# Kernel optimization log

Measured on AMD Instinct MI355X. Metric: run time of the kernel, lower is better.

## Reference

```python
import jax, jax.numpy as jnp
import numpy as np

B, S, HS = 2, 2048, 2048
H, KVH, D = 8, 1, 256
ROPE_BASE = 10000.0


def _rope_cos_sin(position_ids, dim, base=ROPE_BASE):
    # position_ids: (B, S) int -> cos/sin: (B, S, dim)
    inv_freq = 1.0 / (base ** (jnp.arange(0, dim, 2, dtype=jnp.float32) / dim))
    thetas = position_ids.astype(jnp.float32)[..., None] * inv_freq  # (B,S,dim/2)
    emb = jnp.concatenate([thetas, thetas], axis=-1)  # (B,S,dim)
    return jnp.cos(emb), jnp.sin(emb)


def _rotate_half(x):
    x1, x2 = jnp.split(x, 2, axis=-1)
    return jnp.concatenate([-x2, x1], axis=-1)


def _apply_rope(q, k, cos, sin):
    # q,k: (B,h,S,D); cos,sin: (B,S,D) -> unsqueeze head dim
    cos = cos[:, None, :, :]
    sin = sin[:, None, :, :]
    q_emb = q * cos + _rotate_half(q) * sin
    k_emb = k * cos + _rotate_half(k) * sin
    return q_emb, k_emb


def setup_inputs() -> dict:
    key = jax.random.key(0)
    k0, k1, k2, k3, k4 = jax.random.split(key, 5)
    hidden_states = jax.random.normal(k0, (B, S, HS), jnp.float32)
    # causal additive mask: 0 where j<=i, large negative otherwise
    causal = jnp.tril(jnp.ones((S, S), dtype=bool))
    attention_mask = jnp.where(causal, 0.0, -1e9).astype(jnp.float32)
    attention_mask = jnp.broadcast_to(attention_mask[None, None], (B, 1, S, S))
    position_ids = jnp.broadcast_to(jnp.arange(S, dtype=jnp.int32)[None], (B, S))
    scale = 0.02
    Wq = jax.random.normal(k1, (HS, H * D), jnp.float32) * scale
    Wk = jax.random.normal(k2, (HS, KVH * D), jnp.float32) * scale
    Wv = jax.random.normal(k3, (HS, KVH * D), jnp.float32) * scale
    Wo = jax.random.normal(k4, (H * D, HS), jnp.float32) * scale
    return {"hidden_states": hidden_states, "attention_mask": attention_mask,
            "position_ids": position_ids, "Wq": Wq, "Wk": Wk, "Wv": Wv, "Wo": Wo}


def reference(hidden_states, attention_mask, position_ids, Wq, Wk, Wv, Wo):
    bs, seq_len, _ = hidden_states.shape
    q = (hidden_states @ Wq).reshape(bs, seq_len, H, D).transpose(0, 2, 1, 3)     # (B,H,S,D)
    k = (hidden_states @ Wk).reshape(bs, seq_len, KVH, D).transpose(0, 2, 1, 3)   # (B,KVH,S,D)
    v = (hidden_states @ Wv).reshape(bs, seq_len, KVH, D).transpose(0, 2, 1, 3)
    cos, sin = _rope_cos_sin(position_ids, D)
    q, k = _apply_rope(q, k, cos, sin)
    n_rep = H // KVH
    k = jnp.repeat(k, n_rep, axis=1)  # GQA repeat -> (B,H,S,D)
    v = jnp.repeat(v, n_rep, axis=1)
    scores = jnp.einsum('bhqd,bhkd->bhqk', q, k) / jnp.sqrt(jnp.float32(D))
    scores = scores + attention_mask
    attn = jax.nn.softmax(scores.astype(jnp.float32), axis=-1).astype(q.dtype)
    out = jnp.einsum('bhqk,bhkd->bhqd', attn, v)            # (B,H,S,D)
    out = out.transpose(0, 2, 1, 3).reshape(bs, seq_len, H * D)
    return out @ Wo
```

## Files before the change

kernel.cpp:

```cpp
#include <hip/hip_runtime.h>
#include <hip/hip_bf16.h>

typedef __bf16 bf16x8 __attribute__((ext_vector_type(8)));
typedef __bf16 bf16x4 __attribute__((ext_vector_type(4)));
typedef float  f32x4  __attribute__((ext_vector_type(4)));

#define MFMA16(a, b, c) __builtin_amdgcn_mfma_f32_16x16x32_bf16((a), (b), (c), 0, 0, 0)

#define GLOBAL_AS(p) ((const __attribute__((address_space(1))) void*)(p))
#define LDS_AS(p)    ((__attribute__((address_space(3))) void*)(p))

__global__ __launch_bounds__(256) void cvt_bf16_kernel(const float* __restrict__ in,
                                                       __bf16* __restrict__ out)
{
    const int idx = blockIdx.x * 256 + threadIdx.x;
    const float4* p = (const float4*)in + (size_t)idx * 2;
    float4 a = p[0], b = p[1];
    bf16x8 o;
    o[0] = (__bf16)a.x; o[1] = (__bf16)a.y; o[2] = (__bf16)a.z; o[3] = (__bf16)a.w;
    o[4] = (__bf16)b.x; o[5] = (__bf16)b.y; o[6] = (__bf16)b.z; o[7] = (__bf16)b.w;
    ((bf16x8*)out)[idx] = o;
}

__global__ __launch_bounds__(128) void trig_kernel(float2* __restrict__ cs)
{
    const int s = blockIdx.x, i = threadIdx.x;
    const float theta = (float)s * exp2f((float)i * (-13.287712379549449f / 128.f));
    float sn, c;
    sincosf(theta, &sn, &c);
    cs[s * 128 + i] = make_float2(c, sn);
}

__global__ __launch_bounds__(256) void transpose_cvt_kernel(const float* __restrict__ W,
                                                            __bf16* __restrict__ Bt,
                                                            int K, int N)
{
    __shared__ float t[32][33];
    const int n0 = blockIdx.x * 32, k0 = blockIdx.y * 32;
    const int x = threadIdx.x, y = threadIdx.y;
#pragma unroll
    for (int r = 0; r < 4; ++r)
        t[y + r * 8][x] = W[(size_t)(k0 + y + r * 8) * N + n0 + x];
    __syncthreads();
#pragma unroll
    for (int r = 0; r < 4; ++r)
        Bt[(size_t)(n0 + y + r * 8) * K + k0 + x] = (__bf16)t[x][y + r * 8];
}

__global__ __launch_bounds__(256) void vt_kernel(const __bf16* __restrict__ qkv,
                                                 __bf16* __restrict__ vT)
{
    __shared__ __bf16 t[32][33];
    const int s0 = blockIdx.x * 32, d0 = blockIdx.y * 32, b = blockIdx.z;
    const int x = threadIdx.x, y = threadIdx.y;
#pragma unroll
    for (int r = 0; r < 4; ++r)
        t[y + r * 8][x] = qkv[(size_t)(b * 2048 + s0 + y + r * 8) * 2560 + 2304 + d0 + x];
    __syncthreads();
#pragma unroll
    for (int r = 0; r < 4; ++r)
        vT[(size_t)(b * 256 + d0 + y + r * 8) * 2048 + s0 + x] = t[x][y + r * 8];
}

template <typename TC>
__global__ __launch_bounds__(256) void gemm_bt(const __bf16* __restrict__ A,
                                               const __bf16* __restrict__ Bt,
                                               TC* __restrict__ C,
                                               int M, int N, int K)
{
    __shared__ __bf16 As[128 * 32];
    __shared__ __bf16 Bs[128 * 32];

    const int tid  = threadIdx.x;
    const int wave = tid >> 6, lane = tid & 63;
    const int quad = lane >> 4, l16 = lane & 15;
    const int wm = (wave >> 1) * 64, wn = (wave & 1) * 64;
    const int bm = blockIdx.y * 128, bn = blockIdx.x * 128;

    f32x4 acc[4][4] = {};

    for (int k0 = 0; k0 < K; k0 += 32) {
        __syncthreads();
#pragma unroll
        for (int c = 0; c < 2; ++c) {
            const int off = tid * 16 + c * 4096;
            const int row = off >> 6;
            const int kb  = (off & 63) >> 1;
            const __bf16* ga = A  + (size_t)(bm + row) * K + k0 + kb;
            const __bf16* gb = Bt + (size_t)(bn + row) * K + k0 + kb;
            __builtin_amdgcn_global_load_lds(GLOBAL_AS(ga), LDS_AS(As + (off >> 1)), 16, 0, 0);
            __builtin_amdgcn_global_load_lds(GLOBAL_AS(gb), LDS_AS(Bs + (off >> 1)), 16, 0, 0);
        }
        __syncthreads();

        bf16x8 af[4];
#pragma unroll
        for (int mi = 0; mi < 4; ++mi)
            af[mi] = *(const bf16x8*)&As[(wm + mi * 16 + l16) * 32 + quad * 8];
#pragma unroll
        for (int ni = 0; ni < 4; ++ni) {
            bf16x8 bfr = *(const bf16x8*)&Bs[(wn + ni * 16 + l16) * 32 + quad * 8];
#pragma unroll
            for (int mi = 0; mi < 4; ++mi)
                acc[mi][ni] = MFMA16(af[mi], bfr, acc[mi][ni]);
        }
    }
#pragma unroll
    for (int mi = 0; mi < 4; ++mi)
#pragma unroll
        for (int ni = 0; ni < 4; ++ni)
#pragma unroll
            for (int r = 0; r < 4; ++r) {
                int row = bm + wm + mi * 16 + quad * 4 + r;
                int col = bn + wn + ni * 16 + l16;
                C[(size_t)row * N + col] = (TC)acc[mi][ni][r];
            }
}

__global__ __launch_bounds__(256) void rope_kernel(__bf16* __restrict__ qkv,
                                                   const float2* __restrict__ cs)
{
    const int bs = blockIdx.x;
    const int s = bs & 2047;
    const int t = threadIdx.x;
    const float QS = 0.09016843787599907f;

    const int hh = t >> 5, i0 = (t & 31) * 4;
    float2 c0 = cs[s * 128 + i0 + 0], c1 = cs[s * 128 + i0 + 1];
    float2 c2 = cs[s * 128 + i0 + 2], c3 = cs[s * 128 + i0 + 3];

    {
        __bf16* p = qkv + (size_t)bs * 2560 + hh * 256 + i0;
        bf16x4 x1 = *(const bf16x4*)p;
        bf16x4 x2 = *(const bf16x4*)(p + 128);
        bf16x4 o1, o2;
        o1[0] = (__bf16)(((float)x1[0] * c0.x - (float)x2[0] * c0.y) * QS);
        o2[0] = (__bf16)(((float)x2[0] * c0.x + (float)x1[0] * c0.y) * QS);
        o1[1] = (__bf16)(((float)x1[1] * c1.x - (float)x2[1] * c1.y) * QS);
        o2[1] = (__bf16)(((float)x2[1] * c1.x + (float)x1[1] * c1.y) * QS);
        o1[2] = (__bf16)(((float)x1[2] * c2.x - (float)x2[2] * c2.y) * QS);
        o2[2] = (__bf16)(((float)x2[2] * c2.x + (float)x1[2] * c2.y) * QS);
        o1[3] = (__bf16)(((float)x1[3] * c3.x - (float)x2[3] * c3.y) * QS);
        o2[3] = (__bf16)(((float)x2[3] * c3.x + (float)x1[3] * c3.y) * QS);
        *(bf16x4*)p = o1;
        *(bf16x4*)(p + 128) = o2;
    }
    if (t < 32) {
        const int j0 = t * 4;
        float2 d0 = cs[s * 128 + j0 + 0], d1 = cs[s * 128 + j0 + 1];
        float2 d2 = cs[s * 128 + j0 + 2], d3 = cs[s * 128 + j0 + 3];
        __bf16* p = qkv + (size_t)bs * 2560 + 2048 + j0;
        bf16x4 x1 = *(const bf16x4*)p;
        bf16x4 x2 = *(const bf16x4*)(p + 128);
        bf16x4 o1, o2;
        o1[0] = (__bf16)((float)x1[0] * d0.x - (float)x2[0] * d0.y);
        o2[0] = (__bf16)((float)x2[0] * d0.x + (float)x1[0] * d0.y);
        o1[1] = (__bf16)((float)x1[1] * d1.x - (float)x2[1] * d1.y);
        o2[1] = (__bf16)((float)x2[1] * d1.x + (float)x1[1] * d1.y);
        o1[2] = (__bf16)((float)x1[2] * d2.x - (float)x2[2] * d2.y);
        o2[2] = (__bf16)((float)x2[2] * d2.x + (float)x1[2] * d2.y);
        o1[3] = (__bf16)((float)x1[3] * d3.x - (float)x2[3] * d3.y);
        o2[3] = (__bf16)((float)x2[3] * d3.x + (float)x1[3] * d3.y);
        *(bf16x4*)p = o1;
        *(bf16x4*)(p + 128) = o2;
    }
}

__global__ __launch_bounds__(256) void attn_kernel(const __bf16* __restrict__ qkv,
                                                   const __bf16* __restrict__ vTg,
                                                   __bf16* __restrict__ og)
{
    __shared__ __bf16 Ks[64 * 256];
    __shared__ __bf16 Vs[272 * 64];
    __shared__ __bf16 Ps[4][16][68];

    const int b = blockIdx.z, h = blockIdx.y;
    const int qt = (int)gridDim.x - 1 - (int)blockIdx.x;
    const int q0 = qt * 64;
    const int tid  = threadIdx.x;
    const int wave = tid >> 6, lane = tid & 63;
    const int quad = lane >> 4, l16 = lane & 15;
    const int xork = l16 & 7;

    if (tid < 128) {
        bf16x8 one;
#pragma unroll
        for (int e = 0; e < 8; ++e) one[e] = (__bf16)1.0f;
        *(bf16x8*)&Vs[256 * 64 + tid * 8] = one;
    }

    const int qrow = q0 + wave * 16 + l16;
    const __bf16* qptr = qkv + (size_t)(b * 2048 + qrow) * 2560 + h * 256;
    bf16x8 qf[8];
#pragma unroll
    for (int dc = 0; dc < 8; ++dc)
        qf[dc] = *(const bf16x8*)(qptr + dc * 32 + quad * 8);

    f32x4 oacc[17] = {};

    const int kKey0 = tid >> 5;
    const int kC    = (tid & 31) ^ (kKey0 & 7);
    const __bf16* kstage0 = qkv + (size_t)b * 2048 * 2560 + 2048
                          + (size_t)kKey0 * 2560 + kC * 8;
    const int vD0 = tid >> 3;
    const int vC  = (tid & 7) ^ (vD0 & 7);
    const __bf16* vstage0 = vTg + (size_t)b * 256 * 2048 + (size_t)vD0 * 2048 + vC * 8;

    int ckK[8];
#pragma unroll
    for (int dc = 0; dc < 8; ++dc) ckK[dc] = (dc * 4 + quad) ^ xork;
    const int chV0 = quad ^ xork;
    const int chV1 = (4 + quad) ^ xork;

    for (int j0 = 0; j0 <= q0; j0 += 64) {
        __syncthreads();
        const __bf16* kst = kstage0 + (size_t)j0 * 2560;
        const __bf16* vst = vstage0 + j0;
#pragma unroll
        for (int p = 0; p < 8; ++p)
            __builtin_amdgcn_global_load_lds(GLOBAL_AS(kst + (size_t)p * 8 * 2560),
                                             LDS_AS(Ks + tid * 8 + p * 2048), 16, 0, 0);
#pragma unroll
        for (int p = 0; p < 8; ++p)
            __builtin_amdgcn_global_load_lds(GLOBAL_AS(vst + (size_t)p * 32 * 2048),
                                             LDS_AS(Vs + tid * 8 + p * 2048), 16, 0, 0);
        __syncthreads();

        f32x4 sc[4] = {};
#pragma unroll
        for (int nt = 0; nt < 4; ++nt) {
            const __bf16* krow = &Ks[(nt * 16 + l16) * 256];
#pragma unroll
            for (int dc = 0; dc < 8; ++dc) {
                bf16x8 kf = *(const bf16x8*)(krow + ckK[dc] * 8);
                sc[nt] = MFMA16(qf[dc], kf, sc[nt]);
            }
        }
        if (j0 == q0) {
#pragma unroll
            for (int nt = 0; nt < 4; ++nt) {
                int key = j0 + nt * 16 + l16;
#pragma unroll
                for (int r = 0; r < 4; ++r) {
                    int row = q0 + wave * 16 + quad * 4 + r;
                    if (key > row) sc[nt][r] = -1e30f;
                }
            }
        }
#pragma unroll
        for (int nt = 0; nt < 4; ++nt)
#pragma unroll
            for (int r = 0; r < 4; ++r)
                Ps[wave][quad * 4 + r][nt * 16 + l16] = (__bf16)exp2f(sc[nt][r] - 8.f);
        bf16x8 pf0 = *(const bf16x8*)&Ps[wave][l16][quad * 8];
        bf16x8 pf1 = *(const bf16x8*)&Ps[wave][l16][32 + quad * 8];
#pragma unroll
        for (int dt = 0; dt < 17; ++dt) {
            const __bf16* vrow = &Vs[(dt * 16 + l16) * 64];
            bf16x8 vf0 = *(const bf16x8*)(vrow + chV0 * 8);
            bf16x8 vf1 = *(const bf16x8*)(vrow + chV1 * 8);
            oacc[dt] = MFMA16(pf0, vf0, oacc[dt]);
            oacc[dt] = MFMA16(pf1, vf1, oacc[dt]);
        }
    }
    float invl[4];
#pragma unroll
    for (int r = 0; r < 4; ++r) invl[r] = 1.f / oacc[16][r];
#pragma unroll
    for (int dt = 0; dt < 16; ++dt)
#pragma unroll
        for (int r = 0; r < 4; ++r) {
            int row = q0 + wave * 16 + quad * 4 + r;
            int col = h * 256 + dt * 16 + l16;
            og[(size_t)(b * 2048 + row) * 2048 + col] = (__bf16)(oacc[dt][r] * invl[r]);
        }
}

extern "C" void kernel_launch(void* const* d_in, const int* in_sizes, int n_in,
                              void* d_out, int out_size, void* d_ws, size_t ws_size,
                              hipStream_t stream)
{
    (void)in_sizes; (void)n_in; (void)out_size; (void)ws_size;
    const float* hidden = (const float*)d_in[0];
    const float* Wq = (const float*)d_in[3];
    const float* Wk = (const float*)d_in[4];
    const float* Wv = (const float*)d_in[5];
    const float* Wo = (const float*)d_in[6];

    char* ws = (char*)d_ws;
    __bf16* hb    = (__bf16*)(ws);
    __bf16* qkv   = (__bf16*)(ws + (16u << 20));
    __bf16* vTb   = (__bf16*)(ws + (36u << 20));
    __bf16* ob    = (__bf16*)(ws + (38u << 20));
    __bf16* Wqkvt = (__bf16*)(ws + (54u << 20));
    __bf16* Wot   = (__bf16*)(ws + (64u << 20));
    float2* csb   = (float2*)(ws + (72u << 20));
    float* out = (float*)d_out;

    dim3 blk(256);
    dim3 tblk(32, 8);
    cvt_bf16_kernel<<<dim3(4096), blk, 0, stream>>>(hidden, hb);
    trig_kernel<<<dim3(2048), dim3(128), 0, stream>>>(csb);
    transpose_cvt_kernel<<<dim3(64, 64), tblk, 0, stream>>>(Wq, Wqkvt, 2048, 2048);
    transpose_cvt_kernel<<<dim3(8, 64), tblk, 0, stream>>>(Wk, Wqkvt + (size_t)2048 * 2048, 2048, 256);
    transpose_cvt_kernel<<<dim3(8, 64), tblk, 0, stream>>>(Wv, Wqkvt + (size_t)2304 * 2048, 2048, 256);
    transpose_cvt_kernel<<<dim3(64, 64), tblk, 0, stream>>>(Wo, Wot, 2048, 2048);
    gemm_bt<__bf16><<<dim3(20, 32), blk, 0, stream>>>(hb, Wqkvt, qkv, 4096, 2560, 2048);
    rope_kernel<<<dim3(4096), blk, 0, stream>>>(qkv, csb);
    vt_kernel<<<dim3(64, 8, 2), tblk, 0, stream>>>(qkv, vTb);
    attn_kernel<<<dim3(32, 8, 2), blk, 0, stream>>>(qkv, vTb, ob);
    gemm_bt<float><<<dim3(16, 32), blk, 0, stream>>>(ob, Wot, out, 4096, 2048, 2048);
}
```

Baseline: 369.1 us.

## Split attention keys across two blocks with combine pass; fuse transposes and inline RoPE trig

Each attention query tile is split into two blocks that process interleaved 32-key chunks. Each block writes unnormalized partial outputs and row sums, and a new combine kernel adds them and normalizes. The aim is more blocks and smaller LDS per block, for better occupancy and load balance on the causal workload. The four weight transpose launches are merged into one, and the RoPE cos/sin table kernel is replaced by computing sincos inside the rope kernel. In exchange the change adds an extra pass over the attention output and writes partial results in bf16.

```diff
diff --git a/kernel.cpp b/kernel.cpp
--- a/kernel.cpp
+++ b/kernel.cpp
@@ -22,21 +22,22 @@
     ((bf16x8*)out)[idx] = o;
 }
 
-__global__ __launch_bounds__(128) void trig_kernel(float2* __restrict__ cs)
-{
-    const int s = blockIdx.x, i = threadIdx.x;
-    const float theta = (float)s * exp2f((float)i * (-13.287712379549449f / 128.f));
-    float sn, c;
-    sincosf(theta, &sn, &c);
-    cs[s * 128 + i] = make_float2(c, sn);
-}
-
-__global__ __launch_bounds__(256) void transpose_cvt_kernel(const float* __restrict__ W,
-                                                            __bf16* __restrict__ Bt,
-                                                            int K, int N)
+__global__ __launch_bounds__(256) void transpose_all_kernel(const float* __restrict__ Wq,
+                                                            const float* __restrict__ Wk,
+                                                            const float* __restrict__ Wv,
+                                                            const float* __restrict__ Wo,
+                                                            __bf16* __restrict__ Wqkvt,
+                                                            __bf16* __restrict__ Wot)
 {
     __shared__ float t[32][33];
-    const int n0 = blockIdx.x * 32, k0 = blockIdx.y * 32;
+    const int id = blockIdx.x;
+    const float* W; __bf16* dst; int N, loc;
+    if (id < 4096)      { W = Wq; dst = Wqkvt;                        N = 2048; loc = id; }
+    else if (id < 4608) { W = Wk; dst = Wqkvt + (size_t)2048 * 2048;  N = 256;  loc = id - 4096; }
+    else if (id < 5120) { W = Wv; dst = Wqkvt + (size_t)2304 * 2048;  N = 256;  loc = id - 4608; }
+    else                { W = Wo; dst = Wot;                          N = 2048; loc = id - 5120; }
+    const int nb = N >> 5;
+    const int n0 = (loc % nb) * 32, k0 = (loc / nb) * 32;
     const int x = threadIdx.x, y = threadIdx.y;
 #pragma unroll
     for (int r = 0; r < 4; ++r)
@@ -44,7 +45,7 @@
     __syncthreads();
 #pragma unroll
     for (int r = 0; r < 4; ++r)
-        Bt[(size_t)(n0 + y + r * 8) * K + k0 + x] = (__bf16)t[x][y + r * 8];
+        dst[(size_t)(n0 + y + r * 8) * 2048 + k0 + x] = (__bf16)t[x][y + r * 8];
 }
 
 __global__ __launch_bounds__(256) void vt_kernel(const __bf16* __restrict__ qkv,
@@ -117,76 +118,73 @@
             }
 }
 
-__global__ __launch_bounds__(256) void rope_kernel(__bf16* __restrict__ qkv,
-                                                   const float2* __restrict__ cs)
+__global__ __launch_bounds__(256) void rope_kernel(__bf16* __restrict__ qkv)
 {
     const int bs = blockIdx.x;
     const int s = bs & 2047;
     const int t = threadIdx.x;
     const float QS = 0.09016843787599907f;
+    const float NF = -13.287712379549449f / 128.f;
 
     const int hh = t >> 5, i0 = (t & 31) * 4;
-    float2 c0 = cs[s * 128 + i0 + 0], c1 = cs[s * 128 + i0 + 1];
-    float2 c2 = cs[s * 128 + i0 + 2], c3 = cs[s * 128 + i0 + 3];
-
+    float cx[4], sx[4];
+#pragma unroll
+    for (int e = 0; e < 4; ++e) {
+        float th = (float)s * exp2f((float)(i0 + e) * NF);
+        sincosf(th, &sx[e], &cx[e]);
+    }
     {
         __bf16* p = qkv + (size_t)bs * 2560 + hh * 256 + i0;
         bf16x4 x1 = *(const bf16x4*)p;
         bf16x4 x2 = *(const bf16x4*)(p + 128);
         bf16x4 o1, o2;
-        o1[0] = (__bf16)(((float)x1[0] * c0.x - (float)x2[0] * c0.y) * QS);
-        o2[0] = (__bf16)(((float)x2[0] * c0.x + (float)x1[0] * c0.y) * QS);
-        o1[1] = (__bf16)(((float)x1[1] * c1.x - (float)x2[1] * c1.y) * QS);
-        o2[1] = (__bf16)(((float)x2[1] * c1.x + (float)x1[1] * c1.y) * QS);
-        o1[2] = (__bf16)(((float)x1[2] * c2.x - (float)x2[2] * c2.y) * QS);
-        o2[2] = (__bf16)(((float)x2[2] * c2.x + (float)x1[2] * c2.y) * QS);
-        o1[3] = (__bf16)(((float)x1[3] * c3.x - (float)x2[3] * c3.y) * QS);
-        o2[3] = (__bf16)(((float)x2[3] * c3.x + (float)x1[3] * c3.y) * QS);
+#pragma unroll
+        for (int e = 0; e < 4; ++e) {
+            o1[e] = (__bf16)(((float)x1[e] * cx[e] - (float)x2[e] * sx[e]) * QS);
+            o2[e] = (__bf16)(((float)x2[e] * cx[e] + (float)x1[e] * sx[e]) * QS);
+        }
         *(bf16x4*)p = o1;
         *(bf16x4*)(p + 128) = o2;
     }
     if (t < 32) {
-        const int j0 = t * 4;
-        float2 d0 = cs[s * 128 + j0 + 0], d1 = cs[s * 128 + j0 + 1];
-        float2 d2 = cs[s * 128 + j0 + 2], d3 = cs[s * 128 + j0 + 3];
-        __bf16* p = qkv + (size_t)bs * 2560 + 2048 + j0;
+        __bf16* p = qkv + (size_t)bs * 2560 + 2048 + i0;
         bf16x4 x1 = *(const bf16x4*)p;
         bf16x4 x2 = *(const bf16x4*)(p + 128);
         bf16x4 o1, o2;
-        o1[0] = (__bf16)((float)x1[0] * d0.x - (float)x2[0] * d0.y);
-        o2[0] = (__bf16)((float)x2[0] * d0.x + (float)x1[0] * d0.y);
-        o1[1] = (__bf16)((float)x1[1] * d1.x - (float)x2[1] * d1.y);
-        o2[1] = (__bf16)((float)x2[1] * d1.x + (float)x1[1] * d1.y);
-        o1[2] = (__bf16)((float)x1[2] * d2.x - (float)x2[2] * d2.y);
-        o2[2] = (__bf16)((float)x2[2] * d2.x + (float)x1[2] * d2.y);
-        o1[3] = (__bf16)((float)x1[3] * d3.x - (float)x2[3] * d3.y);
-        o2[3] = (__bf16)((float)x2[3] * d3.x + (float)x1[3] * d3.y);
+#pragma unroll
+        for (int e = 0; e < 4; ++e) {
+            o1[e] = (__bf16)((float)x1[e] * cx[e] - (float)x2[e] * sx[e]);
+            o2[e] = (__bf16)((float)x2[e] * cx[e] + (float)x1[e] * sx[e]);
+        }
         *(bf16x4*)p = o1;
         *(bf16x4*)(p + 128) = o2;
     }
 }
 
-__global__ __launch_bounds__(256) void attn_kernel(const __bf16* __restrict__ qkv,
-                                                   const __bf16* __restrict__ vTg,
-                                                   __bf16* __restrict__ og)
-{
-    __shared__ __bf16 Ks[64 * 256];
-    __shared__ __bf16 Vs[272 * 64];
-    __shared__ __bf16 Ps[4][16][68];
+__global__ __launch_bounds__(256, 4) void attn_kernel(const __bf16* __restrict__ qkv,
+                                                      const __bf16* __restrict__ vTg,
+                                                      __bf16* __restrict__ po0,
+                                                      __bf16* __restrict__ po1,
+                                                      float* __restrict__ pl)
+{
+    __shared__ __bf16 Ks[32 * 256];
+    __shared__ __bf16 Vs[272 * 32];
+    __shared__ __bf16 Ps[4][16][36];
 
     const int b = blockIdx.z, h = blockIdx.y;
-    const int qt = (int)gridDim.x - 1 - (int)blockIdx.x;
+    const int qt = 31 - (int)(blockIdx.x >> 1);
+    const int kh = blockIdx.x & 1;
     const int q0 = qt * 64;
     const int tid  = threadIdx.x;
     const int wave = tid >> 6, lane = tid & 63;
     const int quad = lane >> 4, l16 = lane & 15;
     const int xork = l16 & 7;
 
-    if (tid < 128) {
+    if (tid < 64) {
         bf16x8 one;
 #pragma unroll
         for (int e = 0; e < 8; ++e) one[e] = (__bf16)1.0f;
-        *(bf16x8*)&Vs[256 * 64 + tid * 8] = one;
+        *(bf16x8*)&Vs[256 * 32 + tid * 8] = one;
     }
 
     const int qrow = q0 + wave * 16 + l16;
@@ -202,33 +200,32 @@
     const int kC    = (tid & 31) ^ (kKey0 & 7);
     const __bf16* kstage0 = qkv + (size_t)b * 2048 * 2560 + 2048
                           + (size_t)kKey0 * 2560 + kC * 8;
-    const int vD0 = tid >> 3;
-    const int vC  = (tid & 7) ^ (vD0 & 7);
+    const int vD0 = tid >> 2;
+    const int vC  = (tid & 3) ^ (vD0 & 3);
     const __bf16* vstage0 = vTg + (size_t)b * 256 * 2048 + (size_t)vD0 * 2048 + vC * 8;
 
     int ckK[8];
 #pragma unroll
     for (int dc = 0; dc < 8; ++dc) ckK[dc] = (dc * 4 + quad) ^ xork;
-    const int chV0 = quad ^ xork;
-    const int chV1 = (4 + quad) ^ xork;
-
-    for (int j0 = 0; j0 <= q0; j0 += 64) {
+    const int chV = quad ^ (l16 & 3);
+
+    for (int j0 = kh * 32; j0 < q0 + 64; j0 += 64) {
         __syncthreads();
         const __bf16* kst = kstage0 + (size_t)j0 * 2560;
         const __bf16* vst = vstage0 + j0;
 #pragma unroll
-        for (int p = 0; p < 8; ++p)
+        for (int p = 0; p < 4; ++p)
             __builtin_amdgcn_global_load_lds(GLOBAL_AS(kst + (size_t)p * 8 * 2560),
                                              LDS_AS(Ks + tid * 8 + p * 2048), 16, 0, 0);
 #pragma unroll
-        for (int p = 0; p < 8; ++p)
-            __builtin_amdgcn_global_load_lds(GLOBAL_AS(vst + (size_t)p * 32 * 2048),
+        for (int p = 0; p < 4; ++p)
+            __builtin_amdgcn_global_load_lds(GLOBAL_AS(vst + (size_t)p * 64 * 2048),
                                              LDS_AS(Vs + tid * 8 + p * 2048), 16, 0, 0);
         __syncthreads();
 
-        f32x4 sc[4] = {};
-#pragma unroll
-        for (int nt = 0; nt < 4; ++nt) {
+        f32x4 sc[2] = {};
+#pragma unroll
+        for (int nt = 0; nt < 2; ++nt) {
             const __bf16* krow = &Ks[(nt * 16 + l16) * 256];
 #pragma unroll
             for (int dc = 0; dc < 8; ++dc) {
@@ -236,9 +233,9 @@
                 sc[nt] = MFMA16(qf[dc], kf, sc[nt]);
             }
         }
-        if (j0 == q0) {
-#pragma unroll
-            for (int nt = 0; nt < 4; ++nt) {
+        if (j0 >= q0) {
+#pragma unroll
+            for (int nt = 0; nt < 2; ++nt) {
                 int key = j0 + nt * 16 + l16;
 #pragma unroll
                 for (int r = 0; r < 4; ++r) {
@@ -248,32 +245,52 @@
             }
         }
 #pragma unroll
-        for (int nt = 0; nt < 4; ++nt)
+        for (int nt = 0; nt < 2; ++nt)
 #pragma unroll
             for (int r = 0; r < 4; ++r)
                 Ps[wave][quad * 4 + r][nt * 16 + l16] = (__bf16)exp2f(sc[nt][r] - 8.f);
-        bf16x8 pf0 = *(const bf16x8*)&Ps[wave][l16][quad * 8];
-        bf16x8 pf1 = *(const bf16x8*)&Ps[wave][l16][32 + quad * 8];
+        bf16x8 pf = *(const bf16x8*)&Ps[wave][l16][quad * 8];
 #pragma unroll
         for (int dt = 0; dt < 17; ++dt) {
-            const __bf16* vrow = &Vs[(dt * 16 + l16) * 64];
-            bf16x8 vf0 = *(const bf16x8*)(vrow + chV0 * 8);
-            bf16x8 vf1 = *(const bf16x8*)(vrow + chV1 * 8);
-            oacc[dt] = MFMA16(pf0, vf0, oacc[dt]);
-            oacc[dt] = MFMA16(pf1, vf1, oacc[dt]);
-        }
-    }
-    float invl[4];
-#pragma unroll
-    for (int r = 0; r < 4; ++r) invl[r] = 1.f / oacc[16][r];
+            bf16x8 vf = *(const bf16x8*)&Vs[(dt * 16 + l16) * 32 + chV * 8];
+            oacc[dt] = MFMA16(pf, vf, oacc[dt]);
+        }
+    }
+    __bf16* pob = kh ? po1 : po0;
+    const int rowb = q0 + wave * 16 + quad * 4;
 #pragma unroll
     for (int dt = 0; dt < 16; ++dt)
 #pragma unroll
         for (int r = 0; r < 4; ++r) {
-            int row = q0 + wave * 16 + quad * 4 + r;
             int col = h * 256 + dt * 16 + l16;
-            og[(size_t)(b * 2048 + row) * 2048 + col] = (__bf16)(oacc[dt][r] * invl[r]);
-        }
+            pob[(size_t)(b * 2048 + rowb + r) * 2048 + col] = (__bf16)oacc[dt][r];
+        }
+    if (l16 == 0) {
+        float* plp = pl + (size_t)((kh * 2 + b) * 8 + h) * 2048 + rowb;
+#pragma unroll
+        for (int r = 0; r < 4; ++r) plp[r] = oacc[16][r];
+    }
+}
+
+__global__ __launch_bounds__(256) void combine_kernel(__bf16* __restrict__ po0,
+                                                      const __bf16* __restrict__ po1,
+                                                      const float* __restrict__ pl)
+{
+    const int row = blockIdx.x;
+    const int b = row >> 11, s = row & 2047;
+    const int t = threadIdx.x;
+    const int h = (t * 8) >> 8;
+    const float l0 = pl[(size_t)((0 * 2 + b) * 8 + h) * 2048 + s];
+    const float l1 = pl[(size_t)((1 * 2 + b) * 8 + h) * 2048 + s];
+    const float inv = 1.f / (l0 + l1);
+    const size_t idx = (size_t)row * 256 + t;
+    bf16x8 a = ((const bf16x8*)po0)[idx];
+    bf16x8 c = ((const bf16x8*)po1)[idx];
+    bf16x8 o;
+#pragma unroll
+    for (int e = 0; e < 8; ++e)
+        o[e] = (__bf16)(((float)a[e] + (float)c[e]) * inv);
+    ((bf16x8*)po0)[idx] = o;
 }
 
 extern "C" void kernel_launch(void* const* d_in, const int* in_sizes, int n_in,
@@ -294,20 +311,18 @@
     __bf16* ob    = (__bf16*)(ws + (38u << 20));
     __bf16* Wqkvt = (__bf16*)(ws + (54u << 20));
     __bf16* Wot   = (__bf16*)(ws + (64u << 20));
-    float2* csb   = (float2*)(ws + (72u << 20));
+    __bf16* po1   = hb;
+    float*  pl    = (float*)Wqkvt;
     float* out = (float*)d_out;
 
     dim3 blk(256);
     dim3 tblk(32, 8);
     cvt_bf16_kernel<<<dim3(4096), blk, 0, stream>>>(hidden, hb);
-    trig_kernel<<<dim3(2048), dim3(128), 0, stream>>>(csb);
-    transpose_cvt_kernel<<<dim3(64, 64), tblk, 0, stream>>>(Wq, Wqkvt, 2048, 2048);
-    transpose_cvt_kernel<<<dim3(8, 64), tblk, 0, stream>>>(Wk, Wqkvt + (size_t)2048 * 2048, 2048, 256);
-    transpose_cvt_kernel<<<dim3(8, 64), tblk, 0, stream>>>(Wv, Wqkvt + (size_t)2304 * 2048, 2048, 256);
-    transpose_cvt_kernel<<<dim3(64, 64), tblk, 0, stream>>>(Wo, Wot, 2048, 2048);
+    transpose_all_kernel<<<dim3(9216), tblk, 0, stream>>>(Wq, Wk, Wv, Wo, Wqkvt, Wot);
     gemm_bt<__bf16><<<dim3(20, 32), blk, 0, stream>>>(hb, Wqkvt, qkv, 4096, 2560, 2048);
-    rope_kernel<<<dim3(4096), blk, 0, stream>>>(qkv, csb);
+    rope_kernel<<<dim3(4096), blk, 0, stream>>>(qkv);
     vt_kernel<<<dim3(64, 8, 2), tblk, 0, stream>>>(qkv, vTb);
-    attn_kernel<<<dim3(32, 8, 2), blk, 0, stream>>>(qkv, vTb, ob);
+    attn_kernel<<<dim3(64, 8, 2), blk, 0, stream>>>(qkv, vTb, ob, po1, pl);
+    combine_kernel<<<dim3(4096), blk, 0, stream>>>(ob, po1, pl);
     gemm_bt<float><<<dim3(16, 32), blk, 0, stream>>>(ob, Wot, out, 4096, 2048, 2048);
 }
```

Result: slower. 379.5 us (+2.8%).
